# Kernel tuning notes

Measured on AMD Instinct MI355X. Metric: run time of the kernel, lower is better.

The kernel has to match this reference:

```python
import jax, jax.numpy as jnp
import numpy as np

PLOGIT_INIT = 1.5

def setup_inputs() -> dict:
    key = jax.random.key(0)
    B, C, H, W = 32, 256, 64, 64
    x = jax.random.normal(key, (B, C, H, W), dtype=jnp.float32)
    plogit = jnp.full((C,), PLOGIT_INIT, dtype=jnp.float32)  # learned param (post channel-expansion)
    return {"input": x, "plogit": plogit}


def reference(input, plogit):
    B, C = input.shape[0], input.shape[1]
    x = input.reshape(B * C, -1)                       # [B*C, HW]  (to_cw)
    s = jnp.sort(x, axis=-1)                           # per-row full sort
    N = s.shape[1]
    p = jax.nn.sigmoid(plogit)                         # [C]
    # torch: p.view(1,-1).repeat(B,1).view(-1) -> channel-major tiling over batch
    p_full = jnp.tile(p, B)                            # [B*C]
    # torch indexes with int(N * p.data[0] -/+ 0.02): a single scalar column index
    p0 = jax.lax.stop_gradient(p[0])
    i_low = jnp.clip((N * (p0 - 0.02)).astype(jnp.int32), 0, N - 1)
    i_high = jnp.clip((N * (p0 + 0.02)).astype(jnp.int32), 0, N - 1)
    x_low = jax.lax.stop_gradient(jnp.take(s, i_low, axis=1))    # [B*C], detached
    x_high = jax.lax.stop_gradient(jnp.take(s, i_high, axis=1))  # [B*C], detached
    thr = x_low + (x_high - x_low) * p_full            # linear interp, grad flows via p
    thr = thr.reshape(B, C, 1, 1)                      # from_cw
    return jax.nn.relu(input - thr)
```

## Files before the change

### kernel.cpp

```cpp
#include <hip/hip_runtime.h>
#include <math.h>

#define NTHREADS 256
#define WPB      4
#define NELEM    4096
#define EPL      64
#define NREP1    4
#define HSTRIDE  260
#define WAVE_LDS (NREP1 * HSTRIDE)
#define LDSW     (WPB * WAVE_LDS)

typedef float v4f __attribute__((ext_vector_type(4)));

__device__ __forceinline__ unsigned f2ord(float f) {
    unsigned u = __float_as_uint(f);
    return u ^ ((unsigned)((int)u >> 31) | 0x80000000u);
}
__device__ __forceinline__ float ord2f(unsigned k) {
    return __uint_as_float(k ^ (~(unsigned)((int)k >> 31) | 0x80000000u));
}

__device__ __forceinline__ unsigned iscan_dpp(unsigned v) {
    v += (unsigned)__builtin_amdgcn_update_dpp(0, (int)v, 0x111, 0xF, 0xF, false);
    v += (unsigned)__builtin_amdgcn_update_dpp(0, (int)v, 0x112, 0xF, 0xF, false);
    v += (unsigned)__builtin_amdgcn_update_dpp(0, (int)v, 0x114, 0xF, 0xF, false);
    v += (unsigned)__builtin_amdgcn_update_dpp(0, (int)v, 0x118, 0xF, 0xF, false);
    v += (unsigned)__builtin_amdgcn_update_dpp(0, (int)v, 0x142, 0xA, 0xF, false);
    v += (unsigned)__builtin_amdgcn_update_dpp(0, (int)v, 0x143, 0xC, 0xF, false);
    return v;
}

struct Pick2 { unsigned a, b; };

template <int NR>
__device__ __forceinline__ Pick2 wave_pick2(const unsigned* region, int lane,
                                            unsigned rA, unsigned rB) {
    unsigned s0 = 0, s1 = 0, s2 = 0, s3 = 0;
    #pragma unroll
    for (int rep = 0; rep < NR; ++rep) {
        uint4 h = ((const uint4*)(region + rep * HSTRIDE))[lane];
        s0 += h.x; s1 += h.y; s2 += h.z; s3 += h.w;
    }
    unsigned tot = s0 + s1 + s2 + s3;
    unsigned inc = iscan_dpp(tot);
    unsigned ex  = inc - tot;
    unsigned base[4] = {ex, ex + s0, ex + s0 + s1, ex + s0 + s1 + s2};
    unsigned cnt[4]  = {s0, s1, s2, s3};
    unsigned resA = 0, resB = 0;
    bool fA = false, fB = false;
    #pragma unroll
    for (int j = 0; j < 4; ++j) {
        if (rA >= base[j] && rA < base[j] + cnt[j]) {
            resA = ((unsigned)(4 * lane + j) << 12) | (rA - base[j]); fA = true;
        }
        if (rB >= base[j] && rB < base[j] + cnt[j]) {
            resB = ((unsigned)(4 * lane + j) << 12) | (rB - base[j]); fB = true;
        }
    }
    unsigned long long mA = __ballot(fA);
    unsigned long long mB = __ballot(fB);
    Pick2 r;
    r.a = (unsigned)__builtin_amdgcn_readlane((int)resA, (int)(__ffsll((long long)mA) - 1));
    r.b = (unsigned)__builtin_amdgcn_readlane((int)resB, (int)(__ffsll((long long)mB) - 1));
    return r;
}

__global__ void __launch_bounds__(NTHREADS, 4)
xsrelu_kernel(const float* __restrict__ x, const float* __restrict__ plogit,
              float* __restrict__ out, int C, int nrows) {
    __shared__ __align__(16) unsigned hist[LDSW];

    const int tid  = threadIdx.x;
    const int wid  = tid >> 6;
    const int lane = tid & 63;
    const int row  = blockIdx.x * WPB + wid;
    if (row >= nrows) return;

    unsigned* wbase = hist + wid * WAVE_LDS;

    const float4* xr = (const float4*)(x + (size_t)row * NELEM);
    unsigned k[EPL];
    #pragma unroll
    for (int j = 0; j < EPL / 4; ++j) {
        float4 v = xr[j * 64 + lane];
        k[4 * j + 0] = f2ord(v.x);
        k[4 * j + 1] = f2ord(v.y);
        k[4 * j + 2] = f2ord(v.z);
        k[4 * j + 3] = f2ord(v.w);
    }

    float p0 = 1.0f / (1.0f + expf(-plogit[0]));
    float pc = 1.0f / (1.0f + expf(-plogit[row % C]));
    int kLow  = min(max((int)((float)NELEM * (p0 - 0.02f)), 0), NELEM - 1);
    int kHigh = min(max((int)((float)NELEM * (p0 + 0.02f)), 0), NELEM - 1);

    unsigned* my1 = wbase + (lane & (NREP1 - 1)) * HSTRIDE;
    const uint4 z4 = make_uint4(0u, 0u, 0u, 0u);
    #pragma unroll
    for (int r = 0; r < NREP1; ++r)
        ((uint4*)(wbase + r * HSTRIDE))[lane] = z4;
    #pragma unroll
    for (int j = 0; j < EPL; ++j)
        atomicAdd(&my1[k[j] >> 24], 1u);
    Pick2 p1 = wave_pick2<NREP1>(wbase, lane, (unsigned)kLow, (unsigned)kHigh);
    unsigned bA = p1.a >> 12, bB = p1.b >> 12;
    unsigned prefA = bA << 24, rA = p1.a & 0xFFFu;
    unsigned prefB = bB << 24, rB = p1.b & 0xFFFu;
    unsigned known = 0xFF000000u;
    bool diverged = (bA != bB);

    unsigned* myT = wbase;
    unsigned* myB = wbase + HSTRIDE;
    #pragma unroll 1
    for (int shift = 16; shift >= 0; shift -= 8) {
        if (!diverged) {
            ((uint4*)myT)[lane] = z4;
            #pragma unroll
            for (int j = 0; j < EPL; ++j) {
                unsigned kk = k[j];
                if ((kk & known) == prefA)
                    atomicAdd(&myT[(kk >> shift) & 0xFFu], 1u);
            }
            Pick2 p = wave_pick2<1>(myT, lane, rA, rB);
            unsigned cA = p.a >> 12, cB = p.b >> 12;
            prefA |= cA << shift;  rA = p.a & 0xFFFu;
            prefB |= cB << shift;  rB = p.b & 0xFFFu;
            diverged = (cA != cB);
        } else {
            ((uint4*)myT)[lane] = z4;
            ((uint4*)myB)[lane] = z4;
            #pragma unroll
            for (int j = 0; j < EPL; ++j) {
                unsigned kk = k[j];
                unsigned km = kk & known;
                bool isB = (km == prefB);
                if ((km == prefA) | isB)
                    atomicAdd((isB ? myB : myT) + ((kk >> shift) & 0xFFu), 1u);
            }
            unsigned pa = wave_pick2<1>(myT, lane, rA, rA).a;
            unsigned pb = wave_pick2<1>(myB, lane, rB, rB).a;
            prefA |= (pa >> 12) << shift;  rA = pa & 0xFFFu;
            prefB |= (pb >> 12) << shift;  rB = pb & 0xFFFu;
        }
        known |= 0xFFu << shift;
    }

    float xlow  = ord2f(prefA);
    float xhigh = ord2f(prefB);
    float thr = xlow + (xhigh - xlow) * pc;

    v4f* outr = (v4f*)(out + (size_t)row * NELEM);
    #pragma unroll
    for (int j = 0; j < EPL / 4; ++j) {
        v4f o;
        o.x = fmaxf(ord2f(k[4 * j + 0]) - thr, 0.0f);
        o.y = fmaxf(ord2f(k[4 * j + 1]) - thr, 0.0f);
        o.z = fmaxf(ord2f(k[4 * j + 2]) - thr, 0.0f);
        o.w = fmaxf(ord2f(k[4 * j + 3]) - thr, 0.0f);
        __builtin_nontemporal_store(o, outr + j * 64 + lane);
    }
}

extern "C" void kernel_launch(void* const* d_in, const int* in_sizes, int n_in,
                              void* d_out, int out_size, void* d_ws, size_t ws_size,
                              hipStream_t stream) {
    const float* x      = (const float*)d_in[0];
    const float* plogit = (const float*)d_in[1];
    float* out          = (float*)d_out;
    int C    = in_sizes[1];
    int rows = in_sizes[0] / NELEM;
    int grid = (rows + WPB - 1) / WPB;
    xsrelu_kernel<<<grid, NTHREADS, 0, stream>>>(x, plogit, out, C, rows);
}
```

Baseline: 237.6 us.

## Replace last two radix histogram passes with bitwise binary-search counting

Keeps the 8-bit LDS histogram radix select for the top two bytes, then resolves the lower 16 bits of both order statistics with a per-bit binary search. Each step counts keys below a candidate with register compares and reduces both counts together, packed into one word, through a DPP scan. This removes LDS atomics and histogram scans for the low bytes. In exchange it adds 16 serial steps of 128 compares each plus cross-lane reductions.

Result: slower. 268.4 us (+12.9%).

```diff
diff --git a/kernel.cpp b/kernel.cpp
--- a/kernel.cpp
+++ b/kernel.cpp
@@ -106,47 +106,60 @@
     unsigned bA = p1.a >> 12, bB = p1.b >> 12;
     unsigned prefA = bA << 24, rA = p1.a & 0xFFFu;
     unsigned prefB = bB << 24, rB = p1.b & 0xFFFu;
-    unsigned known = 0xFF000000u;
     bool diverged = (bA != bB);
 
     unsigned* myT = wbase;
     unsigned* myB = wbase + HSTRIDE;
-    #pragma unroll 1
-    for (int shift = 16; shift >= 0; shift -= 8) {
+    {
         if (!diverged) {
             ((uint4*)myT)[lane] = z4;
             #pragma unroll
             for (int j = 0; j < EPL; ++j) {
                 unsigned kk = k[j];
-                if ((kk & known) == prefA)
-                    atomicAdd(&myT[(kk >> shift) & 0xFFu], 1u);
+                if ((kk & 0xFF000000u) == prefA)
+                    atomicAdd(&myT[(kk >> 16) & 0xFFu], 1u);
             }
             Pick2 p = wave_pick2<1>(myT, lane, rA, rB);
-            unsigned cA = p.a >> 12, cB = p.b >> 12;
-            prefA |= cA << shift;  rA = p.a & 0xFFFu;
-            prefB |= cB << shift;  rB = p.b & 0xFFFu;
-            diverged = (cA != cB);
+            prefA |= (p.a >> 12) << 16;
+            prefB |= (p.b >> 12) << 16;
         } else {
             ((uint4*)myT)[lane] = z4;
             ((uint4*)myB)[lane] = z4;
             #pragma unroll
             for (int j = 0; j < EPL; ++j) {
                 unsigned kk = k[j];
-                unsigned km = kk & known;
+                unsigned km = kk & 0xFF000000u;
                 bool isB = (km == prefB);
                 if ((km == prefA) | isB)
-                    atomicAdd((isB ? myB : myT) + ((kk >> shift) & 0xFFu), 1u);
+                    atomicAdd((isB ? myB : myT) + ((kk >> 16) & 0xFFu), 1u);
             }
             unsigned pa = wave_pick2<1>(myT, lane, rA, rA).a;
             unsigned pb = wave_pick2<1>(myB, lane, rB, rB).a;
-            prefA |= (pa >> 12) << shift;  rA = pa & 0xFFFu;
-            prefB |= (pb >> 12) << shift;  rB = pb & 0xFFFu;
+            prefA |= (pa >> 12) << 16;
+            prefB |= (pb >> 12) << 16;
         }
-        known |= 0xFFu << shift;
     }
 
-    float xlow  = ord2f(prefA);
-    float xhigh = ord2f(prefB);
+    unsigned pA = prefA, pB = prefB;
+    #pragma unroll 1
+    for (int b = 15; b >= 0; --b) {
+        unsigned cA = pA | (1u << b);
+        unsigned cB = pB | (1u << b);
+        unsigned cntA = 0, cntB = 0;
+        #pragma unroll
+        for (int j = 0; j < EPL; ++j) {
+            cntA += (k[j] < cA) ? 1u : 0u;
+            cntB += (k[j] < cB) ? 1u : 0u;
+        }
+        unsigned packed = cntA | (cntB << 16);
+        unsigned tot = iscan_dpp(packed);
+        unsigned t = (unsigned)__builtin_amdgcn_readlane((int)tot, 63);
+        if ((t & 0xFFFFu) <= (unsigned)kLow)  pA = cA;
+        if ((t >> 16)     <= (unsigned)kHigh) pB = cB;
+    }
+
+    float xlow  = ord2f(pA);
+    float xhigh = ord2f(pB);
     float thr = xlow + (xhigh - xlow) * pc;
 
     v4f* outr = (v4f*)(out + (size_t)row * NELEM);
```

## Replace register-held row with bucket compaction and bitwise rank descent

Applied to the files above, without the earlier changes.

The kernel no longer keeps all 64 keys per lane in registers. It rereads the row from global memory (likely from cache) for the top-byte histogram, for compacting the selected bucket into LDS, and for the final ReLU pass. The remaining 24 bits of the key are then found by a bitwise binary-search descent over the compacted survivors, with a histogram fallback when a bucket exceeds capacity. This cuts register pressure to allow more occupancy, and replaces the three histogram refinement passes with ballot-based compaction, at the cost of extra global reads and 24 serial count-and-scan steps.

Measured after the change: 268.9 us. 1.13x slower.

```diff
diff --git a/kernel.cpp b/kernel.cpp
--- a/kernel.cpp
+++ b/kernel.cpp
@@ -4,10 +4,11 @@
 #define NTHREADS 256
 #define WPB      4
 #define NELEM    4096
-#define EPL      64
 #define NREP1    4
 #define HSTRIDE  260
-#define WAVE_LDS (NREP1 * HSTRIDE)
+#define CAP      1536
+#define MAXS     (CAP / 64)
+#define WAVE_LDS 1536
 #define LDSW     (WPB * WAVE_LDS)
 
 typedef float v4f __attribute__((ext_vector_type(4)));
@@ -65,10 +66,61 @@
     return r;
 }
 
+__device__ __forceinline__ unsigned compact_bucket(const float4* __restrict__ xr,
+                                                   int lane, unsigned bucket,
+                                                   unsigned* cbuf) {
+    unsigned base = 0;
+    #pragma unroll 4
+    for (int j = 0; j < 16; ++j) {
+        float4 v = xr[j * 64 + lane];
+        unsigned kk4[4] = {f2ord(v.x), f2ord(v.y), f2ord(v.z), f2ord(v.w)};
+        #pragma unroll
+        for (int e = 0; e < 4; ++e) {
+            unsigned kk = kk4[e];
+            bool m = (kk >> 24) == bucket;
+            unsigned long long msk = __ballot(m);
+            unsigned pos = base + (unsigned)__popcll(msk & ((1ull << lane) - 1ull));
+            if (m && pos < CAP) cbuf[pos] = kk;
+            base += (unsigned)__popcll(msk);
+        }
+    }
+    return base;
+}
+
+__device__ __forceinline__ void load_surv(const unsigned* cbuf, int lane,
+                                          unsigned cnt, unsigned S[MAXS]) {
+    #pragma unroll
+    for (int j = 0; j < MAXS; ++j) {
+        unsigned idx = (unsigned)(j * 64 + lane);
+        unsigned w = cbuf[idx];
+        S[j] = (idx < cnt) ? w : 0xFFFFFFFFu;
+    }
+}
+
+__device__ __forceinline__ Pick2 descend24(const unsigned S[MAXS], unsigned bucket,
+                                           unsigned rA, unsigned rB) {
+    unsigned pA = bucket << 24, pB = bucket << 24;
+    #pragma unroll 1
+    for (int b = 23; b >= 0; --b) {
+        unsigned cA = pA | (1u << b), cB = pB | (1u << b);
+        unsigned cntA = 0, cntB = 0;
+        #pragma unroll
+        for (int j = 0; j < MAXS; ++j) {
+            cntA += (S[j] < cA) ? 1u : 0u;
+            cntB += (S[j] < cB) ? 1u : 0u;
+        }
+        unsigned tot = iscan_dpp(cntA | (cntB << 16));
+        unsigned t = (unsigned)__builtin_amdgcn_readlane((int)tot, 63);
+        if ((t & 0xFFFFu) <= rA) pA = cA;
+        if ((t >> 16)     <= rB) pB = cB;
+    }
+    Pick2 r; r.a = pA; r.b = pB; return r;
+}
+
 __global__ void __launch_bounds__(NTHREADS, 4)
 xsrelu_kernel(const float* __restrict__ x, const float* __restrict__ plogit,
               float* __restrict__ out, int C, int nrows) {
-    __shared__ __align__(16) unsigned hist[LDSW];
+    __shared__ __align__(16) unsigned lds[LDSW];
 
     const int tid  = threadIdx.x;
     const int wid  = tid >> 6;
@@ -76,87 +128,115 @@
     const int row  = blockIdx.x * WPB + wid;
     if (row >= nrows) return;
 
-    unsigned* wbase = hist + wid * WAVE_LDS;
-
+    unsigned* wbase = lds + wid * WAVE_LDS;
     const float4* xr = (const float4*)(x + (size_t)row * NELEM);
-    unsigned k[EPL];
-    #pragma unroll
-    for (int j = 0; j < EPL / 4; ++j) {
-        float4 v = xr[j * 64 + lane];
-        k[4 * j + 0] = f2ord(v.x);
-        k[4 * j + 1] = f2ord(v.y);
-        k[4 * j + 2] = f2ord(v.z);
-        k[4 * j + 3] = f2ord(v.w);
-    }
 
     float p0 = 1.0f / (1.0f + expf(-plogit[0]));
     float pc = 1.0f / (1.0f + expf(-plogit[row % C]));
     int kLow  = min(max((int)((float)NELEM * (p0 - 0.02f)), 0), NELEM - 1);
     int kHigh = min(max((int)((float)NELEM * (p0 + 0.02f)), 0), NELEM - 1);
 
-    unsigned* my1 = wbase + (lane & (NREP1 - 1)) * HSTRIDE;
     const uint4 z4 = make_uint4(0u, 0u, 0u, 0u);
     #pragma unroll
     for (int r = 0; r < NREP1; ++r)
         ((uint4*)(wbase + r * HSTRIDE))[lane] = z4;
-    #pragma unroll
-    for (int j = 0; j < EPL; ++j)
-        atomicAdd(&my1[k[j] >> 24], 1u);
+    unsigned* my1 = wbase + (lane & (NREP1 - 1)) * HSTRIDE;
+    #pragma unroll
+    for (int j = 0; j < 16; ++j) {
+        float4 v = xr[j * 64 + lane];
+        atomicAdd(&my1[f2ord(v.x) >> 24], 1u);
+        atomicAdd(&my1[f2ord(v.y) >> 24], 1u);
+        atomicAdd(&my1[f2ord(v.z) >> 24], 1u);
+        atomicAdd(&my1[f2ord(v.w) >> 24], 1u);
+    }
     Pick2 p1 = wave_pick2<NREP1>(wbase, lane, (unsigned)kLow, (unsigned)kHigh);
-    unsigned bA = p1.a >> 12, bB = p1.b >> 12;
-    unsigned prefA = bA << 24, rA = p1.a & 0xFFFu;
-    unsigned prefB = bB << 24, rB = p1.b & 0xFFFu;
-    unsigned known = 0xFF000000u;
+    unsigned bA = p1.a >> 12, rA = p1.a & 0xFFFu;
+    unsigned bB = p1.b >> 12, rB = p1.b & 0xFFFu;
     bool diverged = (bA != bB);
 
-    unsigned* myT = wbase;
-    unsigned* myB = wbase + HSTRIDE;
-    #pragma unroll 1
-    for (int shift = 16; shift >= 0; shift -= 8) {
-        if (!diverged) {
+    unsigned keyA = 0, keyB = 0;
+    bool fb = false;
+    if (!diverged) {
+        unsigned cnt = compact_bucket(xr, lane, bA, wbase);
+        if (cnt <= CAP) {
+            unsigned S[MAXS];
+            load_surv(wbase, lane, cnt, S);
+            Pick2 d = descend24(S, bA, rA, rB);
+            keyA = d.a; keyB = d.b;
+        } else fb = true;
+    } else {
+        unsigned cntA = compact_bucket(xr, lane, bA, wbase);
+        if (cntA <= CAP) {
+            unsigned S[MAXS];
+            load_surv(wbase, lane, cntA, S);
+            keyA = descend24(S, bA, rA, rA).a;
+            unsigned cntB = compact_bucket(xr, lane, bB, wbase);
+            if (cntB <= CAP) {
+                load_surv(wbase, lane, cntB, S);
+                keyB = descend24(S, bB, rB, rB).a;
+            } else fb = true;
+        } else fb = true;
+    }
+
+    if (fb) {
+        unsigned* myT = wbase;
+        unsigned* myB = wbase + HSTRIDE;
+        unsigned known = 0xFF000000u;
+        unsigned prefA = bA << 24, prefB = bB << 24;
+        unsigned lrA = rA, lrB = rB;
+        bool div = diverged;
+        #pragma unroll 1
+        for (int shift = 16; shift >= 0; shift -= 8) {
             ((uint4*)myT)[lane] = z4;
-            #pragma unroll
-            for (int j = 0; j < EPL; ++j) {
-                unsigned kk = k[j];
-                if ((kk & known) == prefA)
-                    atomicAdd(&myT[(kk >> shift) & 0xFFu], 1u);
+            if (div) ((uint4*)myB)[lane] = z4;
+            #pragma unroll 1
+            for (int j = 0; j < 16; ++j) {
+                float4 v = xr[j * 64 + lane];
+                unsigned kk4[4] = {f2ord(v.x), f2ord(v.y), f2ord(v.z), f2ord(v.w)};
+                #pragma unroll
+                for (int e = 0; e < 4; ++e) {
+                    unsigned kk = kk4[e];
+                    unsigned km = kk & known;
+                    if (!div) {
+                        if (km == prefA)
+                            atomicAdd(&myT[(kk >> shift) & 0xFFu], 1u);
+                    } else {
+                        bool isB = (km == prefB);
+                        if ((km == prefA) | isB)
+                            atomicAdd((isB ? myB : myT) + ((kk >> shift) & 0xFFu), 1u);
+                    }
+                }
             }
-            Pick2 p = wave_pick2<1>(myT, lane, rA, rB);
-            unsigned cA = p.a >> 12, cB = p.b >> 12;
-            prefA |= cA << shift;  rA = p.a & 0xFFFu;
-            prefB |= cB << shift;  rB = p.b & 0xFFFu;
-            diverged = (cA != cB);
-        } else {
-            ((uint4*)myT)[lane] = z4;
-            ((uint4*)myB)[lane] = z4;
-            #pragma unroll
-            for (int j = 0; j < EPL; ++j) {
-                unsigned kk = k[j];
-                unsigned km = kk & known;
-                bool isB = (km == prefB);
-                if ((km == prefA) | isB)
-                    atomicAdd((isB ? myB : myT) + ((kk >> shift) & 0xFFu), 1u);
+            if (!div) {
+                Pick2 p = wave_pick2<1>(myT, lane, lrA, lrB);
+                unsigned cA = p.a >> 12, cB = p.b >> 12;
+                prefA |= cA << shift;  lrA = p.a & 0xFFFu;
+                prefB |= cB << shift;  lrB = p.b & 0xFFFu;
+                div = (cA != cB);
+            } else {
+                unsigned pa = wave_pick2<1>(myT, lane, lrA, lrA).a;
+                unsigned pb = wave_pick2<1>(myB, lane, lrB, lrB).a;
+                prefA |= (pa >> 12) << shift;  lrA = pa & 0xFFFu;
+                prefB |= (pb >> 12) << shift;  lrB = pb & 0xFFFu;
             }
-            unsigned pa = wave_pick2<1>(myT, lane, rA, rA).a;
-            unsigned pb = wave_pick2<1>(myB, lane, rB, rB).a;
-            prefA |= (pa >> 12) << shift;  rA = pa & 0xFFFu;
-            prefB |= (pb >> 12) << shift;  rB = pb & 0xFFFu;
-        }
-        known |= 0xFFu << shift;
-    }
-
-    float xlow  = ord2f(prefA);
-    float xhigh = ord2f(prefB);
+            known |= 0xFFu << shift;
+        }
+        keyA = prefA; keyB = prefB;
+    }
+
+    float xlow  = ord2f(keyA);
+    float xhigh = ord2f(keyB);
     float thr = xlow + (xhigh - xlow) * pc;
 
     v4f* outr = (v4f*)(out + (size_t)row * NELEM);
     #pragma unroll
-    for (int j = 0; j < EPL / 4; ++j) {
+    for (int j = 0; j < 16; ++j) {
+        float4 v = xr[j * 64 + lane];
         v4f o;
-        o.x = fmaxf(ord2f(k[4 * j + 0]) - thr, 0.0f);
-        o.y = fmaxf(ord2f(k[4 * j + 1]) - thr, 0.0f);
-        o.z = fmaxf(ord2f(k[4 * j + 2]) - thr, 0.0f);
-        o.w = fmaxf(ord2f(k[4 * j + 3]) - thr, 0.0f);
+        o.x = fmaxf(v.x - thr, 0.0f);
+        o.y = fmaxf(v.y - thr, 0.0f);
+        o.z = fmaxf(v.z - thr, 0.0f);
+        o.w = fmaxf(v.w - thr, 0.0f);
         __builtin_nontemporal_store(o, outr + j * 64 + lane);
     }
 }
```

## Process two rows per wave, prefetching the second row during the first row's selection

Applied to the files above, without the earlier changes.

Each wave now handles two consecutive rows. The second row's data is loaded into registers before the first row's histogram radix-select runs, so that global load latency overlaps with LDS work. This doubles the register footprint, so the launch-bounds occupancy hint drops from 4 to 3 blocks, and the grid is halved, which risks lower parallelism and worse tail balance.

New measurement: 242.2 us. No clear change (+1.9%).

```diff
diff --git a/kernel.cpp b/kernel.cpp
--- a/kernel.cpp
+++ b/kernel.cpp
@@ -3,6 +3,7 @@
 
 #define NTHREADS 256
 #define WPB      4
+#define WPW      2
 #define NELEM    4096
 #define EPL      64
 #define NREP1    4
@@ -65,44 +66,19 @@
     return r;
 }
 
-__global__ void __launch_bounds__(NTHREADS, 4)
-xsrelu_kernel(const float* __restrict__ x, const float* __restrict__ plogit,
-              float* __restrict__ out, int C, int nrows) {
-    __shared__ __align__(16) unsigned hist[LDSW];
-
-    const int tid  = threadIdx.x;
-    const int wid  = tid >> 6;
-    const int lane = tid & 63;
-    const int row  = blockIdx.x * WPB + wid;
-    if (row >= nrows) return;
-
-    unsigned* wbase = hist + wid * WAVE_LDS;
-
-    const float4* xr = (const float4*)(x + (size_t)row * NELEM);
-    unsigned k[EPL];
-    #pragma unroll
-    for (int j = 0; j < EPL / 4; ++j) {
-        float4 v = xr[j * 64 + lane];
-        k[4 * j + 0] = f2ord(v.x);
-        k[4 * j + 1] = f2ord(v.y);
-        k[4 * j + 2] = f2ord(v.z);
-        k[4 * j + 3] = f2ord(v.w);
-    }
-
-    float p0 = 1.0f / (1.0f + expf(-plogit[0]));
-    float pc = 1.0f / (1.0f + expf(-plogit[row % C]));
-    int kLow  = min(max((int)((float)NELEM * (p0 - 0.02f)), 0), NELEM - 1);
-    int kHigh = min(max((int)((float)NELEM * (p0 + 0.02f)), 0), NELEM - 1);
-
+struct Keys2 { unsigned a, b; };
+
+__device__ __forceinline__ Keys2 select2(unsigned* wbase, const unsigned k[EPL],
+                                         int lane, unsigned kLow, unsigned kHigh) {
+    const uint4 z4 = make_uint4(0u, 0u, 0u, 0u);
     unsigned* my1 = wbase + (lane & (NREP1 - 1)) * HSTRIDE;
-    const uint4 z4 = make_uint4(0u, 0u, 0u, 0u);
     #pragma unroll
     for (int r = 0; r < NREP1; ++r)
         ((uint4*)(wbase + r * HSTRIDE))[lane] = z4;
     #pragma unroll
     for (int j = 0; j < EPL; ++j)
         atomicAdd(&my1[k[j] >> 24], 1u);
-    Pick2 p1 = wave_pick2<NREP1>(wbase, lane, (unsigned)kLow, (unsigned)kHigh);
+    Pick2 p1 = wave_pick2<NREP1>(wbase, lane, kLow, kHigh);
     unsigned bA = p1.a >> 12, bB = p1.b >> 12;
     unsigned prefA = bA << 24, rA = p1.a & 0xFFFu;
     unsigned prefB = bB << 24, rB = p1.b & 0xFFFu;
@@ -144,12 +120,12 @@
         }
         known |= 0xFFu << shift;
     }
-
-    float xlow  = ord2f(prefA);
-    float xhigh = ord2f(prefB);
-    float thr = xlow + (xhigh - xlow) * pc;
-
-    v4f* outr = (v4f*)(out + (size_t)row * NELEM);
+    Keys2 r; r.a = prefA; r.b = prefB; return r;
+}
+
+__device__ __forceinline__ void epilogue(const unsigned k[EPL], float thr,
+                                         float* __restrict__ orow, int lane) {
+    v4f* outr = (v4f*)orow;
     #pragma unroll
     for (int j = 0; j < EPL / 4; ++j) {
         v4f o;
@@ -159,6 +135,65 @@
         o.w = fmaxf(ord2f(k[4 * j + 3]) - thr, 0.0f);
         __builtin_nontemporal_store(o, outr + j * 64 + lane);
     }
+}
+
+__global__ void __launch_bounds__(NTHREADS, 3)
+xsrelu_kernel(const float* __restrict__ x, const float* __restrict__ plogit,
+              float* __restrict__ out, int C, int nrows) {
+    __shared__ __align__(16) unsigned hist[LDSW];
+
+    const int tid  = threadIdx.x;
+    const int wid  = tid >> 6;
+    const int lane = tid & 63;
+    const int wave = blockIdx.x * WPB + wid;
+    const int row0 = wave * WPW;
+    if (row0 >= nrows) return;
+    const bool have1 = (row0 + 1) < nrows;
+
+    unsigned* wbase = hist + wid * WAVE_LDS;
+    const float4* xr0 = (const float4*)(x + (size_t)row0 * NELEM);
+    const float4* xr1 = (const float4*)(x + (size_t)(row0 + 1) * NELEM);
+
+    unsigned k[EPL];
+    #pragma unroll
+    for (int j = 0; j < EPL / 4; ++j) {
+        float4 v = xr0[j * 64 + lane];
+        k[4 * j + 0] = f2ord(v.x);
+        k[4 * j + 1] = f2ord(v.y);
+        k[4 * j + 2] = f2ord(v.z);
+        k[4 * j + 3] = f2ord(v.w);
+    }
+    float4 nx[EPL / 4];
+    if (have1) {
+        #pragma unroll
+        for (int j = 0; j < EPL / 4; ++j)
+            nx[j] = xr1[j * 64 + lane];
+    }
+    __builtin_amdgcn_sched_barrier(0);
+
+    float p0 = 1.0f / (1.0f + expf(-plogit[0]));
+    unsigned kLow  = (unsigned)min(max((int)((float)NELEM * (p0 - 0.02f)), 0), NELEM - 1);
+    unsigned kHigh = (unsigned)min(max((int)((float)NELEM * (p0 + 0.02f)), 0), NELEM - 1);
+    float pc0 = 1.0f / (1.0f + expf(-plogit[row0 % C]));
+    float pc1 = 1.0f / (1.0f + expf(-plogit[(row0 + 1) % C]));
+
+    Keys2 s0 = select2(wbase, k, lane, kLow, kHigh);
+    float xl0 = ord2f(s0.a), xh0 = ord2f(s0.b);
+    epilogue(k, xl0 + (xh0 - xl0) * pc0, out + (size_t)row0 * NELEM, lane);
+
+    if (!have1) return;
+
+    #pragma unroll
+    for (int j = 0; j < EPL / 4; ++j) {
+        k[4 * j + 0] = f2ord(nx[j].x);
+        k[4 * j + 1] = f2ord(nx[j].y);
+        k[4 * j + 2] = f2ord(nx[j].z);
+        k[4 * j + 3] = f2ord(nx[j].w);
+    }
+
+    Keys2 s1 = select2(wbase, k, lane, kLow, kHigh);
+    float xl1 = ord2f(s1.a), xh1 = ord2f(s1.b);
+    epilogue(k, xl1 + (xh1 - xl1) * pc1, out + (size_t)(row0 + 1) * NELEM, lane);
 }
 
 extern "C" void kernel_launch(void* const* d_in, const int* in_sizes, int n_in,
@@ -169,6 +204,6 @@
     float* out          = (float*)d_out;
     int C    = in_sizes[1];
     int rows = in_sizes[0] / NELEM;
-    int grid = (rows + WPB - 1) / WPB;
+    int grid = (rows + WPB * WPW - 1) / (WPB * WPW);
     xsrelu_kernel<<<grid, NTHREADS, 0, stream>>>(x, plogit, out, C, rows);
 }
```
